# Performance work log

Hardware: AMD Instinct MI355X
Metric: run time of the kernel (lower is better)

Reference implementation:

```python
import jax, jax.numpy as jnp
import numpy as np

D = 256      # hidden_dim
NH = 8       # num_heads
DH = D // NH # head_dim = 32
K = 5        # base_kernel -> NA3D kernel (5,5,5), causal on axis 0 (time)
EPS = 1e-6


def _axis_idx(L, k, causal):
    """Per-axis NATTEN neighbor indices [L, k] and validity mask [L, k]."""
    i = jnp.arange(L)
    o = jnp.arange(k)
    if causal:
        idx = i[:, None] - (k - 1) + o[None, :]   # last k positions incl. self
        mask = idx >= 0
        idx = jnp.clip(idx, 0, L - 1)
    else:
        start = jnp.clip(i - k // 2, 0, L - k)     # window shifts at borders
        idx = start[:, None] + o[None, :]
        mask = jnp.ones((L, k), dtype=bool)
    return idx, mask


def _rmsnorm(x, w):
    return x * jax.lax.rsqrt(jnp.mean(x * x, axis=-1, keepdims=True) + EPS) * w


def _na3d(x, wq, bq, wk, bk, wv, bv, wo, bo):
    # x: [B, T, H, W, D]; neighborhood attention, causal in T.
    B, T, H, W, Dm = x.shape
    q = (x @ wq + bq).reshape(B, T, H, W, NH, DH)
    k = (x @ wk + bk).reshape(B, T, H, W, NH, DH)
    v = (x @ wv + bv).reshape(B, T, H, W, NH, DH)

    tidx, tmask = _axis_idx(T, K, True)
    hidx, _ = _axis_idx(H, K, False)
    widx, _ = _axis_idx(W, K, False)

    # Gather neighbor windows: [B, T, H, W, K, K, K, NH, DH]
    ti = tidx[:, None, None, :, None, None]
    hi = hidx[None, :, None, None, :, None]
    wi = widx[None, None, :, None, None, :]
    kn = k[:, ti, hi, wi].reshape(B, T, H, W, K ** 3, NH, DH)
    vn = v[:, ti, hi, wi].reshape(B, T, H, W, K ** 3, NH, DH)

    # Validity mask (only causal time axis masks anything): [T, H, W, K^3]
    mask = jnp.broadcast_to(tmask[:, None, None, :, None, None],
                            (T, H, W, K, K, K)).reshape(T, H, W, K ** 3)

    logits = jnp.einsum('bthwnd,bthwmnd->bthwnm', q, kn) * (DH ** -0.5)
    logits = jnp.where(mask[None, :, :, :, None, :], logits, -jnp.inf)
    attn = jax.nn.softmax(logits, axis=-1)
    out = jnp.einsum('bthwnm,bthwmnd->bthwnd', attn, vn).reshape(B, T, H, W, Dm)
    return out @ wo + bo


def setup_inputs() -> dict:
    key = jax.random.key(0)
    ks = jax.random.split(key, 14)
    w = lambda k_, shape: jax.random.normal(k_, shape, jnp.float32) * 0.02
    return {
        'x': jax.random.normal(ks[0], (1, 8, 16, 16, D), jnp.float32),
        'norm1_w': jnp.ones((D,), jnp.float32),
        'norm2_w': jnp.ones((D,), jnp.float32),
        'wq': w(ks[1], (D, D)), 'bq': jnp.zeros((D,), jnp.float32),
        'wk': w(ks[2], (D, D)), 'bk': jnp.zeros((D,), jnp.float32),
        'wv': w(ks[3], (D, D)), 'bv': jnp.zeros((D,), jnp.float32),
        'wo': w(ks[4], (D, D)), 'bo': jnp.zeros((D,), jnp.float32),
        'w1': w(ks[5], (D, 4 * D)),
        'w2': w(ks[6], (D, 4 * D)),
        'w3': w(ks[7], (4 * D, D)),
    }


def reference(x, norm1_w, norm2_w, wq, bq, wk, bk, wv, bv, wo, bo, w1, w2, w3):
    # residual NA block
    h = x + _na3d(_rmsnorm(x, norm1_w), wq, bq, wk, bk, wv, bv, wo, bo)
    # residual SwiGLU FFN block
    y = _rmsnorm(h, norm2_w)
    h = h + (jax.nn.silu(y @ w1) * (y @ w2)) @ w3
    return h
```

## Files before the change

kernel.cpp:

```cpp
#include <hip/hip_runtime.h>
#include <hip/hip_bf16.h>

typedef __attribute__((ext_vector_type(8))) __bf16 bf16x8;
typedef __attribute__((ext_vector_type(4))) __bf16 bf16x4;
typedef __attribute__((ext_vector_type(4))) short shortx4;
typedef __attribute__((ext_vector_type(4))) float f32x4;

#define D    256
#define FF   1024
#define NTOK 2048

__device__ __forceinline__ float ldf(const void* p, int i, bool isf32){
  return isf32 ? ((const float*)p)[i] : (float)(((const __bf16*)p)[i]);
}

__device__ __forceinline__ f32x4 mfma16x16x16bf16(bf16x4 a, bf16x4 b, f32x4 c){
#if __has_builtin(__builtin_amdgcn_mfma_f32_16x16x16_bf16)
  return __builtin_amdgcn_mfma_f32_16x16x16_bf16(a, b, c, 0, 0, 0);
#elif __has_builtin(__builtin_amdgcn_mfma_f32_16x16x16bf16_1k)
  return __builtin_amdgcn_mfma_f32_16x16x16bf16_1k(__builtin_bit_cast(shortx4, a),
                                                   __builtin_bit_cast(shortx4, b), c, 0, 0, 0);
#else
  asm volatile("v_mfma_f32_16x16x16_bf16 %0, %1, %2, %0" : "+v"(c) : "v"(a), "v"(b));
  return c;
#endif
}

struct Args {
  const void* x;
  const void* vec[6];
  const void* wsrc[7];
  float* VEC; __bf16* WT;
  __bf16* Qb; __bf16* Kb; __bf16* VTb; __bf16* ATT;
  float* Hb; __bf16* FFH;
  const unsigned int* tagp; void* out;
};

__global__ __launch_bounds__(256) void prep_kernel(Args A){
  __shared__ float tl[32][33];
  bool isf32 = (*A.tagp == 0x3F800000u);
  int b = blockIdx.x, tid = threadIdx.x;

  if (b < 1024){
    const void* src; int Kd, Nd, dstOff, tk, tn;
    if (b < 256){
      int mat = b >> 6, t = b & 63;
      src = A.wsrc[mat]; Kd = 256; Nd = 256; dstOff = mat*65536;
      tk = t >> 3; tn = t & 7;
    } else if (b < 768){
      int mat = (b - 256) >> 8, t = (b - 256) & 255;
      src = A.wsrc[4 + mat]; Kd = 256; Nd = 1024; dstOff = 262144 + mat*262144;
      tk = t >> 5; tn = t & 31;
    } else {
      int t = b - 768;
      src = A.wsrc[6]; Kd = 1024; Nd = 256; dstOff = 786432;
      tk = t >> 3; tn = t & 7;
    }
    int tx = tid & 31, ty = tid >> 5;
    int k0 = tk*32, n0 = tn*32;
    #pragma unroll
    for (int i = 0; i < 4; i++){
      int kk = ty + i*8;
      tl[kk][tx] = ldf(src, (k0 + kk)*Nd + n0 + tx, isf32);
    }
    __syncthreads();
    #pragma unroll
    for (int i = 0; i < 4; i++){
      int nn = ty + i*8;
      A.WT[dstOff + (n0 + nn)*Kd + k0 + tx] = (__bf16)tl[tx][nn];
    }
  } else {
    for (int i = tid; i < 1536; i += 256)
      A.VEC[i] = ldf(A.vec[i >> 8], i & 255, isf32);
  }
}

template<int ROWS>
__device__ __forceinline__ void stageR(const __bf16* __restrict__ src, int strideElems,
                                       __bf16* __restrict__ lds){
  int tid = threadIdx.x;
  #pragma unroll
  for (int c = 0; c < ROWS/8; c++){
    int s = (c*256 + tid) << 4;
    int row = s >> 9, col = s & 511;
    *(float4*)((char*)lds + row*512 + (col ^ ((row & 7) << 4))) =
      *(const float4*)((const char*)src + row*strideElems*2 + col);
  }
}
__device__ __forceinline__ bf16x8 lrd256(const __bf16* __restrict__ lds, int row, int cb){
  return *(const bf16x8*)((const char*)lds + row*512 + (cb ^ ((row & 7) << 4)));
}
__device__ __forceinline__ void stage128(const __bf16* __restrict__ src, int strideElems,
                                         __bf16* __restrict__ lds){
  int tid = threadIdx.x;
  #pragma unroll
  for (int c = 0; c < 4; c++){
    int s = (c*256 + tid) << 4;
    int row = s >> 8, col = s & 255;
    *(float4*)((char*)lds + row*256 + (col ^ ((row & 7) << 4))) =
      *(const float4*)((const char*)src + row*strideElems*2 + col);
  }
}
__device__ __forceinline__ bf16x8 lrd128(const __bf16* __restrict__ lds, int row, int cb){
  return *(const bf16x8*)((const char*)lds + row*256 + (cb ^ ((row & 7) << 4)));
}

__device__ __forceinline__ void stage_norm_rows(const void* src, bool isf32, int m0,
                                                const float* __restrict__ wvec,
                                                __bf16* __restrict__ As){
  int tid = threadIdx.x;
  int wave = tid >> 6, lane = tid & 63;
  float wv[4];
  *(float4*)wv = *(const float4*)&wvec[lane*4];
  #pragma unroll
  for (int i = 0; i < 16; i++){
    int row = wave*16 + i;
    int gbase = (m0 + row)*D + lane*4;
    float v[4];
    if (isf32){
      *(float4*)v = *(const float4*)((const float*)src + gbase);
    } else {
      bf16x4 bv = *(const bf16x4*)((const __bf16*)src + gbase);
      v[0]=(float)bv[0]; v[1]=(float)bv[1]; v[2]=(float)bv[2]; v[3]=(float)bv[3];
    }
    float ss = v[0]*v[0] + v[1]*v[1] + v[2]*v[2] + v[3]*v[3];
    #pragma unroll
    for (int d = 32; d > 0; d >>= 1) ss += __shfl_xor(ss, d, 64);
    float scale = rsqrtf(ss*(1.0f/D) + 1e-6f);
    bf16x4 o;
    #pragma unroll
    for (int j = 0; j < 4; j++) o[j] = (__bf16)(v[j]*scale*wv[j]);
    *(bf16x4*)((char*)As + row*512 + ((lane*8) ^ ((row & 7) << 4))) = o;
  }
}

__device__ __forceinline__ void mfma256(const __bf16* __restrict__ As, const __bf16* __restrict__ Bs,
                                        f32x4 acc[2][2], int wrow, int wcol, int q, int ln){
  #pragma unroll
  for (int ks = 0; ks < 8; ks++){
    int cb = ks*64 + q*16;
    bf16x8 a0 = lrd256(As, wrow*32      + ln, cb);
    bf16x8 a1 = lrd256(As, wrow*32 + 16 + ln, cb);
    bf16x8 b0 = lrd256(Bs, wcol*32      + ln, cb);
    bf16x8 b1 = lrd256(Bs, wcol*32 + 16 + ln, cb);
    acc[0][0] = __builtin_amdgcn_mfma_f32_16x16x32_bf16(a0, b0, acc[0][0], 0, 0, 0);
    acc[0][1] = __builtin_amdgcn_mfma_f32_16x16x32_bf16(a0, b1, acc[0][1], 0, 0, 0);
    acc[1][0] = __builtin_amdgcn_mfma_f32_16x16x32_bf16(a1, b0, acc[1][0], 0, 0, 0);
    acc[1][1] = __builtin_amdgcn_mfma_f32_16x16x32_bf16(a1, b1, acc[1][1], 0, 0, 0);
  }
}

__device__ __forceinline__ void mfma256_m32(const __bf16* __restrict__ As, const __bf16* __restrict__ Bs,
                                            f32x4 acc[2], int wcol, int q, int ln){
  #pragma unroll
  for (int ks = 0; ks < 8; ks++){
    int cb = ks*64 + q*16;
    bf16x8 a0 = lrd256(As, ln,      cb);
    bf16x8 a1 = lrd256(As, 16 + ln, cb);
    bf16x8 b  = lrd256(Bs, wcol*16 + ln, cb);
    acc[0] = __builtin_amdgcn_mfma_f32_16x16x32_bf16(a0, b, acc[0], 0, 0, 0);
    acc[1] = __builtin_amdgcn_mfma_f32_16x16x32_bf16(a1, b, acc[1], 0, 0, 0);
  }
}

#define GEMM_PROLOGUE \
  int tid = threadIdx.x; \
  int wave = tid >> 6, lane = tid & 63; \
  int wrow = wave & 1, wcol = wave >> 1; \
  int q = lane >> 4, ln = lane & 15; \
  (void)tid; \
  f32x4 acc[2][2]; \
  acc[0][0] = (f32x4){0,0,0,0}; acc[0][1] = (f32x4){0,0,0,0}; \
  acc[1][0] = (f32x4){0,0,0,0}; acc[1][1] = (f32x4){0,0,0,0};

__global__ __launch_bounds__(256) void qkv_kernel(Args A){
  __shared__ __align__(16) __bf16 As[64*256];
  __shared__ __align__(16) __bf16 Bs[64*256];
  bool isf32 = (*A.tagp == 0x3F800000u);
  int m0 = blockIdx.x*64;
  int sel = blockIdx.y >> 2, n0 = (blockIdx.y & 3)*64;
  const __bf16* B = A.WT + sel*65536;
  const float* bias = A.VEC + 512 + sel*256;
  GEMM_PROLOGUE
  stage_norm_rows(A.x, isf32, m0, A.VEC, As);
  stageR<64>(B + n0*D, D, Bs);
  __syncthreads();
  mfma256(As, Bs, acc, wrow, wcol, q, ln);
  if (sel < 2){
    __bf16* O = (sel == 0) ? A.Qb : A.Kb;
    #pragma unroll
    for (int c = 0; c < 2; c++){
      int col = n0 + wcol*32 + c*16 + ln;
      float bv = bias[col];
      #pragma unroll
      for (int r = 0; r < 2; r++){
        #pragma unroll
        for (int i = 0; i < 4; i++){
          int m = m0 + wrow*32 + r*16 + q*4 + i;
          O[m*D + col] = (__bf16)(acc[r][c][i] + bv);
        }
      }
    }
  } else {
    #pragma unroll
    for (int c = 0; c < 2; c++){
      int col = n0 + wcol*32 + c*16 + ln;
      float bv = bias[col];
      #pragma unroll
      for (int r = 0; r < 2; r++){
        int mb = m0 + wrow*32 + r*16 + q*4;
        bf16x4 pk;
        #pragma unroll
        for (int i = 0; i < 4; i++) pk[i] = (__bf16)(acc[r][c][i] + bv);
        *(bf16x4*)&A.VTb[col*NTOK + mb] = pk;
      }
    }
  }
}

__global__ __launch_bounds__(256) void attn_kernel(Args A){
  int row = blockIdx.x;
  int tq = row >> 4, hq = row & 15;
  int g  = (blockIdx.y << 2) + (threadIdx.x >> 6);
  int lane = threadIdx.x & 63;
  int ln = lane & 15, qt = lane >> 4;

  int qbase = (tq << 8) + (hq << 4);
  int h0 = min(max(hq - 2, 0), 11);
  int tlo = max(tq - 4, 0);

  bf16x8 qf = *(const bf16x8*)&A.Qb[(qbase + ln)*D + g*32 + qt*8];

  int wstart = min(max(ln - 2, 0), 11);
  float msk[4];
  #pragma unroll
  for (int r = 0; r < 4; r++){
    int wk = qt*4 + r;
    msk[r] = (wk >= wstart && wk <= wstart + 4) ? 0.0f : -INFINITY;
  }

  const float sc = 0.17677669529663687f;
  float m_run = -INFINITY, l_run = 0.0f;
  f32x4 o0 = (f32x4){0,0,0,0}, o1 = (f32x4){0,0,0,0};
  f32x4 zero = (f32x4){0,0,0,0};

  for (int tp = tlo; tp <= tq; tp++){
    #pragma unroll
    for (int hp = 0; hp < 5; hp++){
      int kb0 = (tp << 8) + ((h0 + hp) << 4);
      bf16x8 kf = *(const bf16x8*)&A.Kb[(kb0 + ln)*D + g*32 + qt*8];
      f32x4 s = __builtin_amdgcn_mfma_f32_16x16x32_bf16(kf, qf, zero, 0, 0, 0);
      float sv0 = s[0]*sc + msk[0];
      float sv1 = s[1]*sc + msk[1];
      float sv2 = s[2]*sc + msk[2];
      float sv3 = s[3]*sc + msk[3];
      float tm = fmaxf(fmaxf(sv0, sv1), fmaxf(sv2, sv3));
      tm = fmaxf(tm, __shfl_xor(tm, 16, 64));
      tm = fmaxf(tm, __shfl_xor(tm, 32, 64));
      float mnew = fmaxf(m_run, tm);
      float rs = __expf(m_run - mnew);
      float p0 = __expf(sv0 - mnew), p1 = __expf(sv1 - mnew);
      float p2 = __expf(sv2 - mnew), p3 = __expf(sv3 - mnew);
      bf16x4 pa;
      pa[0] = (__bf16)p0; pa[1] = (__bf16)p1; pa[2] = (__bf16)p2; pa[3] = (__bf16)p3;
      l_run = l_run*rs + (float)pa[0] + (float)pa[1] + (float)pa[2] + (float)pa[3];
      #pragma unroll
      for (int i = 0; i < 4; i++){ o0[i] *= rs; o1[i] *= rs; }
      m_run = mnew;
      bf16x4 v0 = *(const bf16x4*)&A.VTb[(g*32      + ln)*NTOK + kb0 + qt*4];
      bf16x4 v1 = *(const bf16x4*)&A.VTb[(g*32 + 16 + ln)*NTOK + kb0 + qt*4];
      o0 = mfma16x16x16bf16(v0, pa, o0);
      o1 = mfma16x16x16bf16(v1, pa, o1);
    }
  }
  l_run += __shfl_xor(l_run, 16, 64);
  l_run += __shfl_xor(l_run, 32, 64);
  float linv = 1.0f / l_run;
  int obase = (qbase + ln)*D + g*32;
  bf16x4 s0, s1;
  #pragma unroll
  for (int r = 0; r < 4; r++){
    s0[r] = (__bf16)(o0[r] * linv);
    s1[r] = (__bf16)(o1[r] * linv);
  }
  *(bf16x4*)&A.ATT[obase      + qt*4] = s0;
  *(bf16x4*)&A.ATT[obase + 16 + qt*4] = s1;
}

__global__ __launch_bounds__(256) void oproj_kernel(Args A){
  __shared__ __align__(16) __bf16 As[32*256];
  __shared__ __align__(16) __bf16 Bs[64*256];
  bool isf32 = (*A.tagp == 0x3F800000u);
  int m0 = blockIdx.x*32, n0 = blockIdx.y*64;
  int tid = threadIdx.x;
  int wave = tid >> 6, lane = tid & 63;
  int wcol = wave;
  int q = lane >> 4, ln = lane & 15;
  f32x4 acc[2];
  acc[0] = (f32x4){0,0,0,0}; acc[1] = (f32x4){0,0,0,0};
  stageR<32>(A.ATT + m0*D, D, As);
  stageR<64>(A.WT + 196608 + n0*D, D, Bs);
  __syncthreads();
  mfma256_m32(As, Bs, acc, wcol, q, ln);
  int col = n0 + wcol*16 + ln;
  float bv = A.VEC[1280 + col];
  #pragma unroll
  for (int r = 0; r < 2; r++){
    #pragma unroll
    for (int i = 0; i < 4; i++){
      int m = m0 + r*16 + q*4 + i;
      int idx = m*D + col;
      A.Hb[idx] = acc[r][i] + bv + ldf(A.x, idx, isf32);
    }
  }
}

__global__ __launch_bounds__(256) void ffn1_kernel(Args A){
  __shared__ __align__(16) __bf16 As [64*256];
  __shared__ __align__(16) __bf16 B1s[64*128];
  __shared__ __align__(16) __bf16 B2s[64*128];
  const __bf16* W1T = A.WT + 262144;
  const __bf16* W2T = A.WT + 524288;
  int m0 = blockIdx.x*64, n0 = blockIdx.y*64;
  int tid = threadIdx.x;
  int wave = tid >> 6, lane = tid & 63;
  int wrow = wave & 1, wcol = wave >> 1;
  int q = lane >> 4, ln = lane & 15;
  f32x4 acc1[2][2], acc2[2][2];
  #pragma unroll
  for (int r = 0; r < 2; r++)
    #pragma unroll
    for (int c = 0; c < 2; c++){ acc1[r][c] = (f32x4){0,0,0,0}; acc2[r][c] = (f32x4){0,0,0,0}; }

  stage_norm_rows(A.Hb, true, m0, A.VEC + 256, As);

  #pragma unroll
  for (int k0 = 0; k0 < D; k0 += 128){
    if (k0) __syncthreads();
    stage128(W1T + n0*D + k0, D, B1s);
    stage128(W2T + n0*D + k0, D, B2s);
    __syncthreads();
    #pragma unroll
    for (int ks = 0; ks < 4; ks++){
      int cbb = ks*64 + q*16;
      int cba = k0*2 + cbb;
      bf16x8 a0 = lrd256(As,  wrow*32      + ln, cba);
      bf16x8 a1 = lrd256(As,  wrow*32 + 16 + ln, cba);
      bf16x8 p0 = lrd128(B1s, wcol*32      + ln, cbb);
      bf16x8 p1 = lrd128(B1s, wcol*32 + 16 + ln, cbb);
      bf16x8 u0 = lrd128(B2s, wcol*32      + ln, cbb);
      bf16x8 u1 = lrd128(B2s, wcol*32 + 16 + ln, cbb);
      acc1[0][0] = __builtin_amdgcn_mfma_f32_16x16x32_bf16(a0, p0, acc1[0][0], 0,0,0);
      acc1[0][1] = __builtin_amdgcn_mfma_f32_16x16x32_bf16(a0, p1, acc1[0][1], 0,0,0);
      acc1[1][0] = __builtin_amdgcn_mfma_f32_16x16x32_bf16(a1, p0, acc1[1][0], 0,0,0);
      acc1[1][1] = __builtin_amdgcn_mfma_f32_16x16x32_bf16(a1, p1, acc1[1][1], 0,0,0);
      acc2[0][0] = __builtin_amdgcn_mfma_f32_16x16x32_bf16(a0, u0, acc2[0][0], 0,0,0);
      acc2[0][1] = __builtin_amdgcn_mfma_f32_16x16x32_bf16(a0, u1, acc2[0][1], 0,0,0);
      acc2[1][0] = __builtin_amdgcn_mfma_f32_16x16x32_bf16(a1, u0, acc2[1][0], 0,0,0);
      acc2[1][1] = __builtin_amdgcn_mfma_f32_16x16x32_bf16(a1, u1, acc2[1][1], 0,0,0);
    }
  }
  #pragma unroll
  for (int c = 0; c < 2; c++){
    int col = n0 + wcol*32 + c*16 + ln;
    #pragma unroll
    for (int r = 0; r < 2; r++){
      #pragma unroll
      for (int i = 0; i < 4; i++){
        int m = m0 + wrow*32 + r*16 + q*4 + i;
        float gv = acc1[r][c][i], u = acc2[r][c][i];
        float sig = 1.0f / (1.0f + __expf(-gv));
        A.FFH[m*FF + col] = (__bf16)(gv * sig * u);
      }
    }
  }
}

__global__ __launch_bounds__(256) void ffn2_kernel(Args A){
  __shared__ __align__(16) __bf16 As[32*256];
  __shared__ __align__(16) __bf16 Bs[64*256];
  const __bf16* W3T = A.WT + 786432;
  bool isf32 = (*A.tagp == 0x3F800000u);
  int m0 = blockIdx.x*32, n0 = blockIdx.y*64;
  int tid = threadIdx.x;
  int wave = tid >> 6, lane = tid & 63;
  int wcol = wave;
  int q = lane >> 4, ln = lane & 15;
  f32x4 acc[2];
  acc[0] = (f32x4){0,0,0,0}; acc[1] = (f32x4){0,0,0,0};
  #pragma unroll
  for (int k0 = 0; k0 < FF; k0 += 256){
    if (k0) __syncthreads();
    stageR<32>(A.FFH + m0*FF + k0, FF, As);
    stageR<64>(W3T   + n0*FF + k0, FF, Bs);
    __syncthreads();
    mfma256_m32(As, Bs, acc, wcol, q, ln);
  }
  int col = n0 + wcol*16 + ln;
  #pragma unroll
  for (int r = 0; r < 2; r++){
    #pragma unroll
    for (int i = 0; i < 4; i++){
      int m = m0 + r*16 + q*4 + i;
      int idx = m*D + col;
      float val = acc[r][i] + A.Hb[idx];
      if (isf32) ((float*)A.out)[idx] = val;
      else       ((__bf16*)A.out)[idx] = (__bf16)val;
    }
  }
}

extern "C" void kernel_launch(void* const* d_in, const int* in_sizes, int n_in,
                              void* d_out, int out_size, void* d_ws, size_t ws_size,
                              hipStream_t stream){
  char* ws = (char*)d_ws;
  Args A;
  A.VEC  = (float*)(ws + 2097152);
  A.WT   = (__bf16*)(ws + 2097152 + 8192);
  A.Qb   = (__bf16*)(ws + 5251072);
  A.Kb   = A.Qb + NTOK*D;
  A.VTb  = A.Kb + NTOK*D;
  A.ATT  = (__bf16*)(ws + 11542528);
  A.Hb   = (float*)(ws + 12591104);
  A.FFH  = A.Qb;
  A.tagp = (const unsigned int*)d_in[1];
  A.out  = d_out;

  A.x = d_in[0];
  A.vec[0] = d_in[1]; A.vec[1] = d_in[2]; A.vec[2] = d_in[4];
  A.vec[3] = d_in[6]; A.vec[4] = d_in[8]; A.vec[5] = d_in[10];

  A.wsrc[0] = d_in[3];  A.wsrc[1] = d_in[5];  A.wsrc[2] = d_in[7];
  A.wsrc[3] = d_in[9];  A.wsrc[4] = d_in[11]; A.wsrc[5] = d_in[12];
  A.wsrc[6] = d_in[13];

  prep_kernel<<<1025, 256, 0, stream>>>(A);
  qkv_kernel<<<dim3(NTOK/64, 12), 256, 0, stream>>>(A);
  attn_kernel<<<dim3(128, 2), 256, 0, stream>>>(A);
  oproj_kernel<<<dim3(NTOK/32, 4), 256, 0, stream>>>(A);
  ffn1_kernel<<<dim3(NTOK/64, 16), 256, 0, stream>>>(A);
  ffn2_kernel<<<dim3(NTOK/32, 4), 256, 0, stream>>>(A);
}
```

Before: 139.3 us.

## Precompute RMSNorm outputs and row sums upstream instead of per GEMM tile

The first RMSNorm moves into the prep kernel, which writes a normalized bf16 copy of x once, so the QKV GEMM no longer renormalizes the same rows in each of its 12 column-tile blocks. The QKV GEMM switches to 32-row tiles (doubling its grid) and just stages the precomputed rows. The o-proj epilogue now emits per-column-tile partial sums of squares of the residual, so ffn1 can apply the second RMSNorm without a cross-lane reduction. In exchange, prep grows by 2048 blocks, extra workspace buffers are written and read, and o-proj gains LDS reductions and more barriers.

```diff
diff --git a/kernel.cpp b/kernel.cpp
--- a/kernel.cpp
+++ b/kernel.cpp
@@ -30,14 +30,15 @@
   const void* x;
   const void* vec[6];
   const void* wsrc[7];
-  float* VEC; __bf16* WT;
+  float* VEC; __bf16* WT; __bf16* XN;
   __bf16* Qb; __bf16* Kb; __bf16* VTb; __bf16* ATT;
-  float* Hb; __bf16* FFH;
+  float* Hb; float* RSP; __bf16* FFH;
   const unsigned int* tagp; void* out;
 };
 
 __global__ __launch_bounds__(256) void prep_kernel(Args A){
   __shared__ float tl[32][33];
+  __shared__ float red[4];
   bool isf32 = (*A.tagp == 0x3F800000u);
   int b = blockIdx.x, tid = threadIdx.x;
 
@@ -69,6 +70,18 @@
       int nn = ty + i*8;
       A.WT[dstOff + (n0 + nn)*Kd + k0 + tx] = (__bf16)tl[tx][nn];
     }
+  } else if (b < 3072){
+    int tok = b - 1024;
+    int idx = tok*D + tid;
+    float xv = ldf(A.x, idx, isf32);
+    float s = xv*xv;
+    #pragma unroll
+    for (int d = 32; d > 0; d >>= 1) s += __shfl_xor(s, d, 64);
+    if ((tid & 63) == 0) red[tid >> 6] = s;
+    __syncthreads();
+    float tot = red[0]+red[1]+red[2]+red[3];
+    float w = ldf(A.vec[0], tid, isf32);
+    A.XN[idx] = (__bf16)(xv * rsqrtf(tot*(1.0f/D) + 1e-6f) * w);
   } else {
     for (int i = tid; i < 1536; i += 256)
       A.VEC[i] = ldf(A.vec[i >> 8], i & 255, isf32);
@@ -105,31 +118,25 @@
   return *(const bf16x8*)((const char*)lds + row*256 + (cb ^ ((row & 7) << 4)));
 }
 
-__device__ __forceinline__ void stage_norm_rows(const void* src, bool isf32, int m0,
-                                                const float* __restrict__ wvec,
-                                                __bf16* __restrict__ As){
+__device__ __forceinline__ void stage_hb_norm(const float* __restrict__ Hb,
+                                              const float* __restrict__ RSP, int m0,
+                                              const float* __restrict__ w2,
+                                              __bf16* __restrict__ As){
   int tid = threadIdx.x;
   int wave = tid >> 6, lane = tid & 63;
-  float wv[4];
-  *(float4*)wv = *(const float4*)&wvec[lane*4];
-  #pragma unroll
-  for (int i = 0; i < 16; i++){
-    int row = wave*16 + i;
-    int gbase = (m0 + row)*D + lane*4;
-    float v[4];
-    if (isf32){
-      *(float4*)v = *(const float4*)((const float*)src + gbase);
-    } else {
-      bf16x4 bv = *(const bf16x4*)((const __bf16*)src + gbase);
-      v[0]=(float)bv[0]; v[1]=(float)bv[1]; v[2]=(float)bv[2]; v[3]=(float)bv[3];
-    }
-    float ss = v[0]*v[0] + v[1]*v[1] + v[2]*v[2] + v[3]*v[3];
-    #pragma unroll
-    for (int d = 32; d > 0; d >>= 1) ss += __shfl_xor(ss, d, 64);
+  float4 wv = *(const float4*)&w2[lane*4];
+  #pragma unroll
+  for (int c = 0; c < 16; c++){
+    int row = c*4 + wave;
+    int gr = m0 + row;
+    float4 v = *(const float4*)&Hb[gr*D + lane*4];
+    float ss = RSP[gr] + RSP[NTOK + gr] + RSP[2*NTOK + gr] + RSP[3*NTOK + gr];
     float scale = rsqrtf(ss*(1.0f/D) + 1e-6f);
     bf16x4 o;
-    #pragma unroll
-    for (int j = 0; j < 4; j++) o[j] = (__bf16)(v[j]*scale*wv[j]);
+    o[0] = (__bf16)(v.x*scale*wv.x);
+    o[1] = (__bf16)(v.y*scale*wv.y);
+    o[2] = (__bf16)(v.z*scale*wv.z);
+    o[3] = (__bf16)(v.w*scale*wv.w);
     *(bf16x4*)((char*)As + row*512 + ((lane*8) ^ ((row & 7) << 4))) = o;
   }
 }
@@ -163,57 +170,42 @@
   }
 }
 
-#define GEMM_PROLOGUE \
-  int tid = threadIdx.x; \
-  int wave = tid >> 6, lane = tid & 63; \
-  int wrow = wave & 1, wcol = wave >> 1; \
-  int q = lane >> 4, ln = lane & 15; \
-  (void)tid; \
-  f32x4 acc[2][2]; \
-  acc[0][0] = (f32x4){0,0,0,0}; acc[0][1] = (f32x4){0,0,0,0}; \
-  acc[1][0] = (f32x4){0,0,0,0}; acc[1][1] = (f32x4){0,0,0,0};
-
 __global__ __launch_bounds__(256) void qkv_kernel(Args A){
-  __shared__ __align__(16) __bf16 As[64*256];
+  __shared__ __align__(16) __bf16 As[32*256];
   __shared__ __align__(16) __bf16 Bs[64*256];
-  bool isf32 = (*A.tagp == 0x3F800000u);
-  int m0 = blockIdx.x*64;
+  int m0 = blockIdx.x*32;
   int sel = blockIdx.y >> 2, n0 = (blockIdx.y & 3)*64;
   const __bf16* B = A.WT + sel*65536;
   const float* bias = A.VEC + 512 + sel*256;
-  GEMM_PROLOGUE
-  stage_norm_rows(A.x, isf32, m0, A.VEC, As);
+  int tid = threadIdx.x;
+  int wave = tid >> 6, lane = tid & 63;
+  int wcol = wave, q = lane >> 4, ln = lane & 15;
+  f32x4 acc[2];
+  acc[0] = (f32x4){0,0,0,0}; acc[1] = (f32x4){0,0,0,0};
+  stageR<32>(A.XN + m0*D, D, As);
   stageR<64>(B + n0*D, D, Bs);
   __syncthreads();
-  mfma256(As, Bs, acc, wrow, wcol, q, ln);
+  mfma256_m32(As, Bs, acc, wcol, q, ln);
+  int col = n0 + wcol*16 + ln;
+  float bv = bias[col];
   if (sel < 2){
     __bf16* O = (sel == 0) ? A.Qb : A.Kb;
     #pragma unroll
-    for (int c = 0; c < 2; c++){
-      int col = n0 + wcol*32 + c*16 + ln;
-      float bv = bias[col];
+    for (int r = 0; r < 2; r++){
       #pragma unroll
-      for (int r = 0; r < 2; r++){
-        #pragma unroll
-        for (int i = 0; i < 4; i++){
-          int m = m0 + wrow*32 + r*16 + q*4 + i;
-          O[m*D + col] = (__bf16)(acc[r][c][i] + bv);
-        }
+      for (int i = 0; i < 4; i++){
+        int m = m0 + r*16 + q*4 + i;
+        O[m*D + col] = (__bf16)(acc[r][i] + bv);
       }
     }
   } else {
     #pragma unroll
-    for (int c = 0; c < 2; c++){
-      int col = n0 + wcol*32 + c*16 + ln;
-      float bv = bias[col];
+    for (int r = 0; r < 2; r++){
+      int mb = m0 + r*16 + q*4;
+      bf16x4 pk;
       #pragma unroll
-      for (int r = 0; r < 2; r++){
-        int mb = m0 + wrow*32 + r*16 + q*4;
-        bf16x4 pk;
-        #pragma unroll
-        for (int i = 0; i < 4; i++) pk[i] = (__bf16)(acc[r][c][i] + bv);
-        *(bf16x4*)&A.VTb[col*NTOK + mb] = pk;
-      }
+      for (int i = 0; i < 4; i++) pk[i] = (__bf16)(acc[r][i] + bv);
+      *(bf16x4*)&A.VTb[col*NTOK + mb] = pk;
     }
   }
 }
@@ -294,8 +286,7 @@
   int m0 = blockIdx.x*32, n0 = blockIdx.y*64;
   int tid = threadIdx.x;
   int wave = tid >> 6, lane = tid & 63;
-  int wcol = wave;
-  int q = lane >> 4, ln = lane & 15;
+  int wcol = wave, q = lane >> 4, ln = lane & 15;
   f32x4 acc[2];
   acc[0] = (f32x4){0,0,0,0}; acc[1] = (f32x4){0,0,0,0};
   stageR<32>(A.ATT + m0*D, D, As);
@@ -303,15 +294,40 @@
   __syncthreads();
   mfma256_m32(As, Bs, acc, wcol, q, ln);
   int col = n0 + wcol*16 + ln;
+  int lc  = wcol*16 + ln;
   float bv = A.VEC[1280 + col];
+  float vals[2][4];
   #pragma unroll
   for (int r = 0; r < 2; r++){
     #pragma unroll
     for (int i = 0; i < 4; i++){
       int m = m0 + r*16 + q*4 + i;
       int idx = m*D + col;
-      A.Hb[idx] = acc[r][i] + bv + ldf(A.x, idx, isf32);
-    }
+      float v = acc[r][i] + bv + ldf(A.x, idx, isf32);
+      A.Hb[idx] = v;
+      vals[r][i] = v;
+    }
+  }
+  __syncthreads();
+  float* rsq = (float*)As;
+  #pragma unroll
+  for (int r = 0; r < 2; r++)
+    #pragma unroll
+    for (int i = 0; i < 4; i++)
+      rsq[(r*16 + q*4 + i)*64 + lc] = vals[r][i]*vals[r][i];
+  __syncthreads();
+  int rrow = tid >> 3, s8 = tid & 7;
+  float p = 0.0f;
+  #pragma unroll
+  for (int j = 0; j < 8; j++) p += rsq[rrow*64 + s8*8 + j];
+  float* r2 = rsq + 2048;
+  r2[rrow*8 + s8] = p;
+  __syncthreads();
+  if (tid < 32){
+    float t = 0.0f;
+    #pragma unroll
+    for (int s = 0; s < 8; s++) t += r2[tid*8 + s];
+    A.RSP[blockIdx.y*NTOK + m0 + tid] = t;
   }
 }
 
@@ -332,7 +348,7 @@
     #pragma unroll
     for (int c = 0; c < 2; c++){ acc1[r][c] = (f32x4){0,0,0,0}; acc2[r][c] = (f32x4){0,0,0,0}; }
 
-  stage_norm_rows(A.Hb, true, m0, A.VEC + 256, As);
+  stage_hb_norm(A.Hb, A.RSP, m0, A.VEC + 256, As);
 
   #pragma unroll
   for (int k0 = 0; k0 < D; k0 += 128){
@@ -384,8 +400,7 @@
   int m0 = blockIdx.x*32, n0 = blockIdx.y*64;
   int tid = threadIdx.x;
   int wave = tid >> 6, lane = tid & 63;
-  int wcol = wave;
-  int q = lane >> 4, ln = lane & 15;
+  int wcol = wave, q = lane >> 4, ln = lane & 15;
   f32x4 acc[2];
   acc[0] = (f32x4){0,0,0,0}; acc[1] = (f32x4){0,0,0,0};
   #pragma unroll
@@ -417,11 +432,13 @@
   Args A;
   A.VEC  = (float*)(ws + 2097152);
   A.WT   = (__bf16*)(ws + 2097152 + 8192);
+  A.XN   = (__bf16*)(ws + 4202496);
   A.Qb   = (__bf16*)(ws + 5251072);
   A.Kb   = A.Qb + NTOK*D;
   A.VTb  = A.Kb + NTOK*D;
   A.ATT  = (__bf16*)(ws + 11542528);
   A.Hb   = (float*)(ws + 12591104);
+  A.RSP  = (float*)(ws + 14688256);
   A.FFH  = A.Qb;
   A.tagp = (const unsigned int*)d_in[1];
   A.out  = d_out;
@@ -434,8 +451,8 @@
   A.wsrc[3] = d_in[9];  A.wsrc[4] = d_in[11]; A.wsrc[5] = d_in[12];
   A.wsrc[6] = d_in[13];
 
-  prep_kernel<<<1025, 256, 0, stream>>>(A);
-  qkv_kernel<<<dim3(NTOK/64, 12), 256, 0, stream>>>(A);
+  prep_kernel<<<3073, 256, 0, stream>>>(A);
+  qkv_kernel<<<dim3(NTOK/32, 12), 256, 0, stream>>>(A);
   attn_kernel<<<dim3(128, 2), 256, 0, stream>>>(A);
   oproj_kernel<<<dim3(NTOK/32, 4), 256, 0, stream>>>(A);
   ffn1_kernel<<<dim3(NTOK/64, 16), 256, 0, stream>>>(A);
```

New measurement: 133.3 us. 1.05x faster.
